# Kernel tuning notes

Hardware: AMD Instinct MI355X
Metric: run time of the kernel (lower is better)

## Reference

```python
import jax, jax.numpy as jnp
import numpy as np

N_NODES = 50000
N_EDGES = 800000
D_IN = 128
D_OUT = 128


def setup_inputs() -> dict:
    key = jax.random.key(0)
    k1, k2, k3, k4, k5 = jax.random.split(key, 5)
    x = jax.random.normal(k1, (N_NODES, D_IN), dtype=jnp.float32)
    src = jax.random.randint(k2, (N_EDGES,), 0, N_NODES, dtype=jnp.int32)
    dst = jax.random.randint(k3, (N_EDGES,), 0, N_NODES, dtype=jnp.int32)
    # nn.Linear(in_feats, out_feats): weight [out, in], bias [out]
    W = jax.random.normal(k4, (D_OUT, D_IN), dtype=jnp.float32) / np.sqrt(D_IN)
    b = jax.random.normal(k5, (D_OUT,), dtype=jnp.float32) * 0.01
    return {"x": x, "src": src, "dst": dst, "W": W, "b": b}


def reference(x, src, dst, W, b):
    # copy_u('h','m') + sum reduce: h_dst = sum_{e:(u->v)} x[u]
    msgs = x[src]  # [E, D_IN] gather of source features
    h = jax.ops.segment_sum(msgs, dst, num_segments=N_NODES)  # [N, D_IN]
    # linear: h @ W.T + b ; dropout_rate=0.0 -> identity
    out = jnp.einsum('nd,od->no', h, W) + b
    return out
```

## Files before the change

kernel.cpp:

```cpp
#include <hip/hip_runtime.h>

#define N_NODES 50000
#define N_EDGES 800000
#define D 128
#define NB 782
#define SORT_CAP 2048

typedef __attribute__((ext_vector_type(8))) short bf16x8;
typedef __attribute__((ext_vector_type(4))) float floatx4;

__device__ __forceinline__ unsigned short f2bf(float f) {
  unsigned u = __builtin_bit_cast(unsigned, f);
  unsigned r = u + 0x7FFFu + ((u >> 16) & 1u);
  return (unsigned short)(r >> 16);
}
__device__ __forceinline__ float bf2f_lo(unsigned u) {
  return __builtin_bit_cast(float, u << 16);
}
__device__ __forceinline__ float bf2f_hi(unsigned u) {
  return __builtin_bit_cast(float, u & 0xFFFF0000u);
}

#define BIN_T 512
#define BIN_CHUNK 3200
#define BIN_BLOCKS 250

__global__ __launch_bounds__(BIN_T) void bin_agg(
    const int* __restrict__ src, const int* __restrict__ dst,
    int* __restrict__ bcursor, unsigned* __restrict__ ebuf, int cap) {
  __shared__ unsigned stage[BIN_CHUNK];
  __shared__ unsigned short stageb[BIN_CHUNK];
  __shared__ int hcnt[NB];
  __shared__ int hstart[NB];
  __shared__ int hcur[NB];
  __shared__ int hgbase[NB];
  __shared__ int wsums[8];

  int t = threadIdx.x;
  int e0 = blockIdx.x * BIN_CHUNK;
  for (int i = t; i < NB; i += BIN_T) hcnt[i] = 0;
  __syncthreads();

  unsigned pk[7];
  short bk[7];
#pragma unroll
  for (int j = 0; j < 7; ++j) {
    int idx = j * BIN_T + t;
    bk[j] = -1;
    if (idx < BIN_CHUNK) {
      int e = e0 + idx;
      int d = dst[e];
      int s = src[e];
      pk[j] = ((unsigned)s << 6) | (unsigned)(d & 63);
      bk[j] = (short)(d >> 6);
      atomicAdd(&hcnt[d >> 6], 1);
    }
  }
  __syncthreads();

  int i0 = 2 * t, i1 = 2 * t + 1;
  int c0 = (i0 < NB) ? hcnt[i0] : 0;
  int c1 = (i1 < NB) ? hcnt[i1] : 0;
  int s2 = c0 + c1;
  int incl = s2;
  int lane = t & 63, wid = t >> 6;
#pragma unroll
  for (int off = 1; off < 64; off <<= 1) {
    int n = __shfl_up(incl, off);
    if (lane >= off) incl += n;
  }
  if (lane == 63) wsums[wid] = incl;
  __syncthreads();
  int wbase = 0;
  for (int w2 = 0; w2 < wid; ++w2) wbase += wsums[w2];
  int base = wbase + incl - s2;
  if (i0 < NB) { hstart[i0] = base;      hcur[i0] = base; }
  if (i1 < NB) { hstart[i1] = base + c0; hcur[i1] = base + c0; }
  __syncthreads();

  for (int i = t; i < NB; i += BIN_T) {
    int c = hcnt[i];
    hgbase[i] = c ? atomicAdd(&bcursor[i * 16], c) : 0;
  }
#pragma unroll
  for (int j = 0; j < 7; ++j) {
    if (bk[j] >= 0) {
      int p = atomicAdd(&hcur[bk[j]], 1);
      stage[p] = pk[j];
      stageb[p] = (unsigned short)bk[j];
    }
  }
  __syncthreads();

  for (int i = t; i < BIN_CHUNK; i += BIN_T) {
    int b = stageb[i];
    int g = hgbase[b] + (i - hstart[b]);
    if (g < cap) ebuf[(size_t)b * cap + g] = stage[i];
  }
}

#define LDA 136
__global__ __launch_bounds__(256) void gemm_xw(
    const float* __restrict__ x, const float* __restrict__ W,
    unsigned short* __restrict__ y) {
  __shared__ unsigned short As[64 * LDA];
  __shared__ unsigned short Ws[128 * LDA];

  int t = threadIdx.x;
  int row0 = blockIdx.x * 64;

  for (int i = t; i < 2048; i += 256) {
    int r = i >> 5;
    int c4 = (i & 31) * 4;
    int gr = row0 + r;
    float4 v = (gr < N_NODES) ? *(const float4*)(x + (size_t)gr * D + c4)
                              : float4{0.f, 0.f, 0.f, 0.f};
    unsigned short* p = &As[r * LDA + c4];
    p[0] = f2bf(v.x); p[1] = f2bf(v.y); p[2] = f2bf(v.z); p[3] = f2bf(v.w);
  }
  for (int i = t; i < 4096; i += 256) {
    int r = i >> 5;
    int c4 = (i & 31) * 4;
    float4 wv = *(const float4*)(W + (size_t)r * D + c4);
    unsigned short* q = &Ws[r * LDA + c4];
    q[0] = f2bf(wv.x); q[1] = f2bf(wv.y); q[2] = f2bf(wv.z); q[3] = f2bf(wv.w);
  }
  __syncthreads();

  int w = t >> 6;
  int lane = t & 63;
  int ln = lane & 15;
  int quad = lane >> 4;

  floatx4 acc[8];
#pragma unroll
  for (int n = 0; n < 8; ++n) acc[n] = floatx4{0.f, 0.f, 0.f, 0.f};

#pragma unroll
  for (int ks = 0; ks < 4; ++ks) {
    int kc = ks * 32 + quad * 8;
    bf16x8 a = *(const bf16x8*)&As[(w * 16 + ln) * LDA + kc];
#pragma unroll
    for (int n = 0; n < 8; ++n) {
      bf16x8 bf = *(const bf16x8*)&Ws[(n * 16 + ln) * LDA + kc];
      acc[n] = __builtin_amdgcn_mfma_f32_16x16x32_bf16(a, bf, acc[n], 0, 0, 0);
    }
  }

  int gr0 = row0 + w * 16 + quad * 4;
#pragma unroll
  for (int n = 0; n < 8; ++n) {
    int gc = n * 16 + ln;
#pragma unroll
    for (int r = 0; r < 4; ++r) {
      int gr = gr0 + r;
      if (gr < N_NODES) y[(size_t)gr * D + gc] = f2bf(acc[n][r]);
    }
  }
}

__global__ __launch_bounds__(256) void gather_sorted(
    const unsigned short* __restrict__ y, const unsigned* __restrict__ ebuf,
    const int* __restrict__ bcursor, const float* __restrict__ bias,
    float* __restrict__ out, int cap) {
  __shared__ int cnts[64];
  __shared__ int curs[64];
  __shared__ int starts[65];
  __shared__ int sorted[SORT_CAP];

  int b = blockIdx.x;
  int t = threadIdx.x;
  if (t < 64) cnts[t] = 0;
  __syncthreads();

  int cnt = bcursor[b * 16];
  if (cnt > cap) cnt = cap;
  if (cnt > SORT_CAP) cnt = SORT_CAP;
  const unsigned* eb = ebuf + (size_t)b * cap;

  for (int i = t; i < cnt; i += 256) atomicAdd(&cnts[eb[i] & 63u], 1);
  __syncthreads();

  if (t < 64) {
    int c = cnts[t];
    int v = c;
#pragma unroll
    for (int off = 1; off < 64; off <<= 1) {
      int n = __shfl_up(v, off);
      if (t >= off) v += n;
    }
    starts[t] = v - c;
    curs[t] = v - c;
    if (t == 63) starts[64] = v;
  }
  __syncthreads();

  for (int i = t; i < cnt; i += 256) {
    unsigned u = eb[i];
    int p = atomicAdd(&curs[u & 63u], 1);
    sorted[p] = (int)(u >> 6);
  }
  __syncthreads();

  int wv = t >> 6;
  int lane = t & 63;
  int g = lane >> 4;
  int l = lane & 15;
  for (int n = wv; n < 64; n += 4) {
    int node = b * 64 + n;
    int beg = starts[n];
    int end = starts[n + 1];
    float acc[8] = {0.f, 0.f, 0.f, 0.f, 0.f, 0.f, 0.f, 0.f};
    int i = beg + g;
    for (; i + 12 < end; i += 16) {
      int s0 = sorted[i];
      int s1 = sorted[i + 4];
      int s2 = sorted[i + 8];
      int s3 = sorted[i + 12];
      uint4 u0 = *(const uint4*)(y + (size_t)s0 * D + l * 8);
      uint4 u1 = *(const uint4*)(y + (size_t)s1 * D + l * 8);
      uint4 u2 = *(const uint4*)(y + (size_t)s2 * D + l * 8);
      uint4 u3 = *(const uint4*)(y + (size_t)s3 * D + l * 8);
      acc[0] += (bf2f_lo(u0.x) + bf2f_lo(u1.x)) + (bf2f_lo(u2.x) + bf2f_lo(u3.x));
      acc[1] += (bf2f_hi(u0.x) + bf2f_hi(u1.x)) + (bf2f_hi(u2.x) + bf2f_hi(u3.x));
      acc[2] += (bf2f_lo(u0.y) + bf2f_lo(u1.y)) + (bf2f_lo(u2.y) + bf2f_lo(u3.y));
      acc[3] += (bf2f_hi(u0.y) + bf2f_hi(u1.y)) + (bf2f_hi(u2.y) + bf2f_hi(u3.y));
      acc[4] += (bf2f_lo(u0.z) + bf2f_lo(u1.z)) + (bf2f_lo(u2.z) + bf2f_lo(u3.z));
      acc[5] += (bf2f_hi(u0.z) + bf2f_hi(u1.z)) + (bf2f_hi(u2.z) + bf2f_hi(u3.z));
      acc[6] += (bf2f_lo(u0.w) + bf2f_lo(u1.w)) + (bf2f_lo(u2.w) + bf2f_lo(u3.w));
      acc[7] += (bf2f_hi(u0.w) + bf2f_hi(u1.w)) + (bf2f_hi(u2.w) + bf2f_hi(u3.w));
    }
    for (; i < end; i += 4) {
      int s = sorted[i];
      uint4 u = *(const uint4*)(y + (size_t)s * D + l * 8);
      acc[0] += bf2f_lo(u.x); acc[1] += bf2f_hi(u.x);
      acc[2] += bf2f_lo(u.y); acc[3] += bf2f_hi(u.y);
      acc[4] += bf2f_lo(u.z); acc[5] += bf2f_hi(u.z);
      acc[6] += bf2f_lo(u.w); acc[7] += bf2f_hi(u.w);
    }
#pragma unroll
    for (int j = 0; j < 8; ++j) {
      acc[j] += __shfl_xor(acc[j], 16);
      acc[j] += __shfl_xor(acc[j], 32);
    }
    if (g == 0 && node < N_NODES) {
      const float* bp = bias + l * 8;
      float4 r0 = {acc[0] + bp[0], acc[1] + bp[1], acc[2] + bp[2], acc[3] + bp[3]};
      float4 r1 = {acc[4] + bp[4], acc[5] + bp[5], acc[6] + bp[6], acc[7] + bp[7]};
      float* op = out + (size_t)node * D + l * 8;
      *(float4*)op = r0;
      *(float4*)(op + 4) = r1;
    }
  }
}

__global__ __launch_bounds__(256) void hist_kernel(
    const int* __restrict__ dst, int* __restrict__ counts) {
  int e = blockIdx.x * 256 + threadIdx.x;
  if (e < N_EDGES) atomicAdd(&counts[dst[e]], 1);
}

#define SBLK 196
__global__ __launch_bounds__(256) void reduce_kernel(
    const int* __restrict__ counts, int* __restrict__ blockSums) {
  int i = blockIdx.x * 256 + threadIdx.x;
  int v = (i < N_NODES) ? counts[i] : 0;
#pragma unroll
  for (int off = 32; off; off >>= 1) v += __shfl_down(v, off);
  __shared__ int ws[4];
  int lane = threadIdx.x & 63, wid = threadIdx.x >> 6;
  if (lane == 0) ws[wid] = v;
  __syncthreads();
  if (threadIdx.x == 0) blockSums[blockIdx.x] = ws[0] + ws[1] + ws[2] + ws[3];
}

__global__ __launch_bounds__(256) void scan_kernel2(
    const int* __restrict__ counts, const int* __restrict__ blockSums,
    int* __restrict__ offsets, int* __restrict__ cursor) {
  int b = blockIdx.x;
  int t = threadIdx.x;
  int lane = t & 63, wid = t >> 6;
  int pv = (t < b) ? blockSums[t] : 0;
#pragma unroll
  for (int off = 32; off; off >>= 1) pv += __shfl_down(pv, off);
  __shared__ int ws[4];
  __shared__ int wsum[4];
  __shared__ int base_s;
  if (lane == 0) ws[wid] = pv;
  __syncthreads();
  if (t == 0) base_s = ws[0] + ws[1] + ws[2] + ws[3];
  int i = b * 256 + t;
  int c = (i < N_NODES) ? counts[i] : 0;
  int v = c;
#pragma unroll
  for (int off = 1; off < 64; off <<= 1) {
    int n = __shfl_up(v, off);
    if (lane >= off) v += n;
  }
  if (lane == 63) wsum[wid] = v;
  __syncthreads();
  int wbase = 0;
  for (int w2 = 0; w2 < wid; ++w2) wbase += wsum[w2];
  int excl = base_s + wbase + v - c;
  if (i < N_NODES) {
    offsets[i] = excl;
    cursor[i] = excl;
    if (i == N_NODES - 1) offsets[N_NODES] = excl + c;
  }
}

__global__ __launch_bounds__(256) void fill_kernel(
    const int* __restrict__ src, const int* __restrict__ dst,
    int* __restrict__ cursor, int* __restrict__ esrc) {
  int e = blockIdx.x * 256 + threadIdx.x;
  if (e >= N_EDGES) return;
  int pos = atomicAdd(&cursor[dst[e]], 1);
  esrc[pos] = src[e];
}

__global__ __launch_bounds__(256) void gather_ybf_kernel(
    const unsigned short* __restrict__ y, const int* __restrict__ esrc,
    const int* __restrict__ offsets, const float* __restrict__ bias,
    float* __restrict__ out) {
  int node = blockIdx.x * 4 + (threadIdx.x >> 6);
  if (node >= N_NODES) return;
  int lane = threadIdx.x & 63;
  int g = lane >> 4;
  int l = lane & 15;
  int beg = offsets[node];
  int end = offsets[node + 1];
  float acc[8] = {0.f, 0.f, 0.f, 0.f, 0.f, 0.f, 0.f, 0.f};
  int i = beg + g;
  for (; i + 4 < end; i += 8) {
    int s0 = esrc[i];
    int s1 = esrc[i + 4];
    uint4 u0 = *(const uint4*)(y + (size_t)s0 * D + l * 8);
    uint4 u1 = *(const uint4*)(y + (size_t)s1 * D + l * 8);
    acc[0] += bf2f_lo(u0.x) + bf2f_lo(u1.x);
    acc[1] += bf2f_hi(u0.x) + bf2f_hi(u1.x);
    acc[2] += bf2f_lo(u0.y) + bf2f_lo(u1.y);
    acc[3] += bf2f_hi(u0.y) + bf2f_hi(u1.y);
    acc[4] += bf2f_lo(u0.z) + bf2f_lo(u1.z);
    acc[5] += bf2f_hi(u0.z) + bf2f_hi(u1.z);
    acc[6] += bf2f_lo(u0.w) + bf2f_lo(u1.w);
    acc[7] += bf2f_hi(u0.w) + bf2f_hi(u1.w);
  }
  if (i < end) {
    int s = esrc[i];
    uint4 u = *(const uint4*)(y + (size_t)s * D + l * 8);
    acc[0] += bf2f_lo(u.x); acc[1] += bf2f_hi(u.x);
    acc[2] += bf2f_lo(u.y); acc[3] += bf2f_hi(u.y);
    acc[4] += bf2f_lo(u.z); acc[5] += bf2f_hi(u.z);
    acc[6] += bf2f_lo(u.w); acc[7] += bf2f_hi(u.w);
  }
#pragma unroll
  for (int j = 0; j < 8; ++j) {
    acc[j] += __shfl_xor(acc[j], 16);
    acc[j] += __shfl_xor(acc[j], 32);
  }
  if (g == 0) {
    const float* bp = bias + l * 8;
    float4 r0 = {acc[0] + bp[0], acc[1] + bp[1], acc[2] + bp[2], acc[3] + bp[3]};
    float4 r1 = {acc[4] + bp[4], acc[5] + bp[5], acc[6] + bp[6], acc[7] + bp[7]};
    float* op = out + (size_t)node * D + l * 8;
    *(float4*)op = r0;
    *(float4*)(op + 4) = r1;
  }
}

__global__ __launch_bounds__(256) void scatter_kernel(
    const float* __restrict__ x, const int* __restrict__ src,
    const int* __restrict__ dst, float* __restrict__ out) {
  int gtid = blockIdx.x * 256 + threadIdx.x;
  int e = gtid >> 6;
  int lane = threadIdx.x & 63;
  if (e >= N_EDGES) return;
  float2 v = ((const float2*)(x + (size_t)src[e] * D))[lane];
  float* orow = out + (size_t)dst[e] * D + lane * 2;
  atomicAdd(orow + 0, v.x);
  atomicAdd(orow + 1, v.y);
}

__global__ __launch_bounds__(256) void transform_kernel(
    float* __restrict__ out, const float* __restrict__ W,
    const float* __restrict__ bias) {
  constexpr int RPB = 64;
  constexpr int HP = 132;
  __shared__ float Hs[RPB][HP];
  int t = threadIdx.x;
  int row0 = blockIdx.x * RPB;
  int nr = min(RPB, N_NODES - row0);
  {
    const float4* g = (const float4*)(out + (size_t)row0 * D);
    for (int i = t; i < nr * (D / 4); i += 256) {
      int r = i >> 5;
      int c = (i & 31) * 4;
      *(float4*)&Hs[r][c] = g[i];
    }
  }
  __syncthreads();
  int tx = t & 15;
  int ty = t >> 4;
  int r0 = ty * 4;
  for (int half = 0; half < 2; ++half) {
    int oc0 = half * 64 + tx * 4;
    const float* Wb = W + (size_t)oc0 * D;
    float4 a0 = {0.f, 0.f, 0.f, 0.f}, a1 = {0.f, 0.f, 0.f, 0.f};
    float4 a2 = {0.f, 0.f, 0.f, 0.f}, a3 = {0.f, 0.f, 0.f, 0.f};
#pragma unroll 8
    for (int k = 0; k < D; k += 4) {
      float4 w0 = *(const float4*)(Wb + 0 * D + k);
      float4 w1 = *(const float4*)(Wb + 1 * D + k);
      float4 w2 = *(const float4*)(Wb + 2 * D + k);
      float4 w3 = *(const float4*)(Wb + 3 * D + k);
      float4 h0 = *(const float4*)&Hs[r0 + 0][k];
      float4 h1 = *(const float4*)&Hs[r0 + 1][k];
      float4 h2 = *(const float4*)&Hs[r0 + 2][k];
      float4 h3 = *(const float4*)&Hs[r0 + 3][k];
#define DOT(hv, wv) fmaf((hv).w, (wv).w, fmaf((hv).z, (wv).z, fmaf((hv).y, (wv).y, (hv).x * (wv).x)))
      a0.x += DOT(h0, w0); a0.y += DOT(h0, w1); a0.z += DOT(h0, w2); a0.w += DOT(h0, w3);
      a1.x += DOT(h1, w0); a1.y += DOT(h1, w1); a1.z += DOT(h1, w2); a1.w += DOT(h1, w3);
      a2.x += DOT(h2, w0); a2.y += DOT(h2, w1); a2.z += DOT(h2, w2); a2.w += DOT(h2, w3);
      a3.x += DOT(h3, w0); a3.y += DOT(h3, w1); a3.z += DOT(h3, w2); a3.w += DOT(h3, w3);
#undef DOT
    }
    float4 bv = *(const float4*)(bias + oc0);
    a0.x += bv.x; a0.y += bv.y; a0.z += bv.z; a0.w += bv.w;
    a1.x += bv.x; a1.y += bv.y; a1.z += bv.z; a1.w += bv.w;
    a2.x += bv.x; a2.y += bv.y; a2.z += bv.z; a2.w += bv.w;
    a3.x += bv.x; a3.y += bv.y; a3.z += bv.z; a3.w += bv.w;
    if (r0 + 0 < nr) *(float4*)(out + (size_t)(row0 + r0 + 0) * D + oc0) = a0;
    if (r0 + 1 < nr) *(float4*)(out + (size_t)(row0 + r0 + 1) * D + oc0) = a1;
    if (r0 + 2 < nr) *(float4*)(out + (size_t)(row0 + r0 + 2) * D + oc0) = a2;
    if (r0 + 3 < nr) *(float4*)(out + (size_t)(row0 + r0 + 3) * D + oc0) = a3;
  }
}

extern "C" void kernel_launch(void* const* d_in, const int* in_sizes, int n_in,
                              void* d_out, int out_size, void* d_ws, size_t ws_size,
                              hipStream_t stream) {
  const float* x = (const float*)d_in[0];
  const int* src = (const int*)d_in[1];
  const int* dst = (const int*)d_in[2];
  const float* W = (const float*)d_in[3];
  const float* b = (const float*)d_in[4];
  float* out = (float*)d_out;

  const size_t ybytes = (size_t)N_NODES * D * sizeof(unsigned short);
  const size_t bcbytes = (size_t)NB * 16 * sizeof(int);

  long long avail = (long long)ws_size - (long long)ybytes - (long long)bcbytes;
  int cap = 0;
  if (avail > 0) {
    long long c = avail / (4LL * NB);
    cap = (c > SORT_CAP) ? SORT_CAP : (int)c;
  }

  if (cap >= 1344) {
    unsigned short* y = (unsigned short*)d_ws;
    int* bcursor = (int*)((char*)d_ws + ybytes);
    unsigned* ebuf = (unsigned*)((char*)bcursor + bcbytes);

    hipMemsetAsync(bcursor, 0, bcbytes, stream);
    bin_agg<<<BIN_BLOCKS, BIN_T, 0, stream>>>(src, dst, bcursor, ebuf, cap);
    gemm_xw<<<NB, 256, 0, stream>>>(x, W, y);
    gather_sorted<<<NB, 256, 0, stream>>>(y, ebuf, bcursor, b, out, cap);
    return;
  }

  const size_t A = 50048;
  const size_t head_ints = 3 * A + 256 + (size_t)N_EDGES;
  const size_t need_csr = head_ints * sizeof(int) + ybytes;

  if (ws_size >= need_csr) {
    int* counts     = (int*)d_ws;
    int* offsets    = counts + A;
    int* cursor     = offsets + A;
    int* blockSums  = cursor + A;
    int* esrc       = blockSums + 256;
    unsigned short* y = (unsigned short*)(esrc + N_EDGES);

    hipMemsetAsync(counts, 0, N_NODES * sizeof(int), stream);
    hist_kernel<<<(N_EDGES + 255) / 256, 256, 0, stream>>>(dst, counts);
    reduce_kernel<<<SBLK, 256, 0, stream>>>(counts, blockSums);
    scan_kernel2<<<SBLK, 256, 0, stream>>>(counts, blockSums, offsets, cursor);
    fill_kernel<<<(N_EDGES + 255) / 256, 256, 0, stream>>>(src, dst, cursor, esrc);
    gemm_xw<<<NB, 256, 0, stream>>>(x, W, y);
    gather_ybf_kernel<<<(N_NODES + 3) / 4, 256, 0, stream>>>(y, esrc, offsets, b, out);
  } else {
    hipMemsetAsync(out, 0, (size_t)N_NODES * D * sizeof(float), stream);
    scatter_kernel<<<N_EDGES / 4, 256, 0, stream>>>(x, src, dst, out);
    transform_kernel<<<(N_NODES + 63) / 64, 256, 0, stream>>>(out, W, b);
  }
}
```

Measured before the change: 152.8 us.

## Fuse edge binning and bf16 GEMM into one heterogeneous prep kernel

Merges the bin_agg and gemm_xw launches into a single prep_kernel whose first NB blocks do the x·W^T MFMA GEMM and whose remaining blocks bin edges by destination block, sharing LDS through a union. The binning blocks are resized to 256 threads and 2048 edges each. The aim is to remove one kernel launch and its serialization and let the independent GEMM and binning work overlap across CUs. The standalone gemm_xw is kept for the fallback path. The union sizes LDS for the larger GEMM layout, which may lower occupancy of the binning blocks.

Result: no change. 150.4 us (-1.6%).

```diff
diff --git a/kernel.cpp b/kernel.cpp
--- a/kernel.cpp
+++ b/kernel.cpp
@@ -21,140 +21,163 @@
   return __builtin_bit_cast(float, u & 0xFFFF0000u);
 }
 
-#define BIN_T 512
-#define BIN_CHUNK 3200
-#define BIN_BLOCKS 250
-
-__global__ __launch_bounds__(BIN_T) void bin_agg(
+#define LDA 136
+#define BIN_T 256
+#define BIN_CHUNK 2048
+#define BIN_BLOCKS 391
+
+struct BinShm {
+  unsigned stage[BIN_CHUNK];
+  unsigned short stageb[BIN_CHUNK];
+  int hcnt[NB];
+  int hstart[NB];
+  int hcur[NB];
+  int hgbase[NB];
+  int wsums[4];
+  int tot;
+};
+struct GemmShm {
+  unsigned short As[64 * LDA];
+  unsigned short Ws[128 * LDA];
+};
+union PrepShm {
+  BinShm bin;
+  GemmShm gemm;
+};
+
+__global__ __launch_bounds__(256) void prep_kernel(
+    const float* __restrict__ x, const float* __restrict__ W,
+    unsigned short* __restrict__ y,
     const int* __restrict__ src, const int* __restrict__ dst,
     int* __restrict__ bcursor, unsigned* __restrict__ ebuf, int cap) {
-  __shared__ unsigned stage[BIN_CHUNK];
-  __shared__ unsigned short stageb[BIN_CHUNK];
-  __shared__ int hcnt[NB];
-  __shared__ int hstart[NB];
-  __shared__ int hcur[NB];
-  __shared__ int hgbase[NB];
-  __shared__ int wsums[8];
-
+  __shared__ PrepShm shm;
   int t = threadIdx.x;
-  int e0 = blockIdx.x * BIN_CHUNK;
-  for (int i = t; i < NB; i += BIN_T) hcnt[i] = 0;
-  __syncthreads();
-
-  unsigned pk[7];
-  short bk[7];
-#pragma unroll
-  for (int j = 0; j < 7; ++j) {
-    int idx = j * BIN_T + t;
-    bk[j] = -1;
-    if (idx < BIN_CHUNK) {
-      int e = e0 + idx;
-      int d = dst[e];
-      int s = src[e];
-      pk[j] = ((unsigned)s << 6) | (unsigned)(d & 63);
-      bk[j] = (short)(d >> 6);
-      atomicAdd(&hcnt[d >> 6], 1);
-    }
-  }
-  __syncthreads();
-
-  int i0 = 2 * t, i1 = 2 * t + 1;
-  int c0 = (i0 < NB) ? hcnt[i0] : 0;
-  int c1 = (i1 < NB) ? hcnt[i1] : 0;
-  int s2 = c0 + c1;
-  int incl = s2;
-  int lane = t & 63, wid = t >> 6;
-#pragma unroll
-  for (int off = 1; off < 64; off <<= 1) {
-    int n = __shfl_up(incl, off);
-    if (lane >= off) incl += n;
-  }
-  if (lane == 63) wsums[wid] = incl;
-  __syncthreads();
-  int wbase = 0;
-  for (int w2 = 0; w2 < wid; ++w2) wbase += wsums[w2];
-  int base = wbase + incl - s2;
-  if (i0 < NB) { hstart[i0] = base;      hcur[i0] = base; }
-  if (i1 < NB) { hstart[i1] = base + c0; hcur[i1] = base + c0; }
-  __syncthreads();
-
-  for (int i = t; i < NB; i += BIN_T) {
-    int c = hcnt[i];
-    hgbase[i] = c ? atomicAdd(&bcursor[i * 16], c) : 0;
-  }
-#pragma unroll
-  for (int j = 0; j < 7; ++j) {
-    if (bk[j] >= 0) {
-      int p = atomicAdd(&hcur[bk[j]], 1);
-      stage[p] = pk[j];
-      stageb[p] = (unsigned short)bk[j];
-    }
-  }
-  __syncthreads();
-
-  for (int i = t; i < BIN_CHUNK; i += BIN_T) {
-    int b = stageb[i];
-    int g = hgbase[b] + (i - hstart[b]);
-    if (g < cap) ebuf[(size_t)b * cap + g] = stage[i];
-  }
-}
-
-#define LDA 136
-__global__ __launch_bounds__(256) void gemm_xw(
-    const float* __restrict__ x, const float* __restrict__ W,
-    unsigned short* __restrict__ y) {
-  __shared__ unsigned short As[64 * LDA];
-  __shared__ unsigned short Ws[128 * LDA];
-
-  int t = threadIdx.x;
-  int row0 = blockIdx.x * 64;
-
-  for (int i = t; i < 2048; i += 256) {
-    int r = i >> 5;
-    int c4 = (i & 31) * 4;
-    int gr = row0 + r;
-    float4 v = (gr < N_NODES) ? *(const float4*)(x + (size_t)gr * D + c4)
-                              : float4{0.f, 0.f, 0.f, 0.f};
-    unsigned short* p = &As[r * LDA + c4];
-    p[0] = f2bf(v.x); p[1] = f2bf(v.y); p[2] = f2bf(v.z); p[3] = f2bf(v.w);
-  }
-  for (int i = t; i < 4096; i += 256) {
-    int r = i >> 5;
-    int c4 = (i & 31) * 4;
-    float4 wv = *(const float4*)(W + (size_t)r * D + c4);
-    unsigned short* q = &Ws[r * LDA + c4];
-    q[0] = f2bf(wv.x); q[1] = f2bf(wv.y); q[2] = f2bf(wv.z); q[3] = f2bf(wv.w);
-  }
-  __syncthreads();
-
-  int w = t >> 6;
-  int lane = t & 63;
-  int ln = lane & 15;
-  int quad = lane >> 4;
-
-  floatx4 acc[8];
-#pragma unroll
-  for (int n = 0; n < 8; ++n) acc[n] = floatx4{0.f, 0.f, 0.f, 0.f};
-
-#pragma unroll
-  for (int ks = 0; ks < 4; ++ks) {
-    int kc = ks * 32 + quad * 8;
-    bf16x8 a = *(const bf16x8*)&As[(w * 16 + ln) * LDA + kc];
+
+  if (blockIdx.x < NB) {
+    unsigned short* As = shm.gemm.As;
+    unsigned short* Ws = shm.gemm.Ws;
+    int row0 = blockIdx.x * 64;
+
+    for (int i = t; i < 2048; i += 256) {
+      int r = i >> 5;
+      int c4 = (i & 31) * 4;
+      int gr = row0 + r;
+      float4 v = (gr < N_NODES) ? *(const float4*)(x + (size_t)gr * D + c4)
+                                : float4{0.f, 0.f, 0.f, 0.f};
+      unsigned short* p = &As[r * LDA + c4];
+      p[0] = f2bf(v.x); p[1] = f2bf(v.y); p[2] = f2bf(v.z); p[3] = f2bf(v.w);
+    }
+    for (int i = t; i < 4096; i += 256) {
+      int r = i >> 5;
+      int c4 = (i & 31) * 4;
+      float4 wv = *(const float4*)(W + (size_t)r * D + c4);
+      unsigned short* q = &Ws[r * LDA + c4];
+      q[0] = f2bf(wv.x); q[1] = f2bf(wv.y); q[2] = f2bf(wv.z); q[3] = f2bf(wv.w);
+    }
+    __syncthreads();
+
+    int w = t >> 6;
+    int lane = t & 63;
+    int ln = lane & 15;
+    int quad = lane >> 4;
+
+    floatx4 acc[8];
+#pragma unroll
+    for (int n = 0; n < 8; ++n) acc[n] = floatx4{0.f, 0.f, 0.f, 0.f};
+
+#pragma unroll
+    for (int ks = 0; ks < 4; ++ks) {
+      int kc = ks * 32 + quad * 8;
+      bf16x8 a = *(const bf16x8*)&As[(w * 16 + ln) * LDA + kc];
+#pragma unroll
+      for (int n = 0; n < 8; ++n) {
+        bf16x8 bf = *(const bf16x8*)&Ws[(n * 16 + ln) * LDA + kc];
+        acc[n] = __builtin_amdgcn_mfma_f32_16x16x32_bf16(a, bf, acc[n], 0, 0, 0);
+      }
+    }
+
+    int gr0 = row0 + w * 16 + quad * 4;
 #pragma unroll
     for (int n = 0; n < 8; ++n) {
-      bf16x8 bf = *(const bf16x8*)&Ws[(n * 16 + ln) * LDA + kc];
-      acc[n] = __builtin_amdgcn_mfma_f32_16x16x32_bf16(a, bf, acc[n], 0, 0, 0);
-    }
-  }
-
-  int gr0 = row0 + w * 16 + quad * 4;
-#pragma unroll
-  for (int n = 0; n < 8; ++n) {
-    int gc = n * 16 + ln;
-#pragma unroll
-    for (int r = 0; r < 4; ++r) {
-      int gr = gr0 + r;
-      if (gr < N_NODES) y[(size_t)gr * D + gc] = f2bf(acc[n][r]);
+      int gc = n * 16 + ln;
+#pragma unroll
+      for (int r = 0; r < 4; ++r) {
+        int gr = gr0 + r;
+        if (gr < N_NODES) y[(size_t)gr * D + gc] = f2bf(acc[n][r]);
+      }
+    }
+  } else {
+    BinShm& B = shm.bin;
+    int blk = blockIdx.x - NB;
+    int e0 = blk * BIN_CHUNK;
+    for (int i = t; i < NB; i += BIN_T) B.hcnt[i] = 0;
+    __syncthreads();
+
+    unsigned pk[8];
+    short bk[8];
+#pragma unroll
+    for (int j = 0; j < 8; ++j) {
+      int e = e0 + j * BIN_T + t;
+      bk[j] = -1;
+      if (e < N_EDGES) {
+        int d = dst[e];
+        int s = src[e];
+        pk[j] = ((unsigned)s << 6) | (unsigned)(d & 63);
+        bk[j] = (short)(d >> 6);
+        atomicAdd(&B.hcnt[d >> 6], 1);
+      }
+    }
+    __syncthreads();
+
+    int c4[4];
+    int s4 = 0;
+    int base4 = t * 4;
+#pragma unroll
+    for (int j = 0; j < 4; ++j) {
+      int idx = base4 + j;
+      c4[j] = (idx < NB) ? B.hcnt[idx] : 0;
+      s4 += c4[j];
+    }
+    int incl = s4;
+    int lane = t & 63, wid = t >> 6;
+#pragma unroll
+    for (int off = 1; off < 64; off <<= 1) {
+      int n = __shfl_up(incl, off);
+      if (lane >= off) incl += n;
+    }
+    if (lane == 63) B.wsums[wid] = incl;
+    __syncthreads();
+    int wbase = 0;
+    for (int w2 = 0; w2 < wid; ++w2) wbase += B.wsums[w2];
+    int run = wbase + incl - s4;
+#pragma unroll
+    for (int j = 0; j < 4; ++j) {
+      int idx = base4 + j;
+      if (idx < NB) { B.hstart[idx] = run; B.hcur[idx] = run; }
+      run += c4[j];
+    }
+    if (t == BIN_T - 1) B.tot = run;
+    __syncthreads();
+
+    for (int i = t; i < NB; i += BIN_T) {
+      int c = B.hcnt[i];
+      B.hgbase[i] = c ? atomicAdd(&bcursor[i * 16], c) : 0;
+    }
+#pragma unroll
+    for (int j = 0; j < 8; ++j) {
+      if (bk[j] >= 0) {
+        int p = atomicAdd(&B.hcur[bk[j]], 1);
+        B.stage[p] = pk[j];
+        B.stageb[p] = (unsigned short)bk[j];
+      }
+    }
+    __syncthreads();
+
+    int tot = B.tot;
+    for (int i = t; i < tot; i += BIN_T) {
+      int b = B.stageb[i];
+      int g = B.hgbase[b] + (i - B.hstart[b]);
+      if (g < cap) ebuf[(size_t)b * cap + g] = B.stage[i];
     }
   }
 }
@@ -318,6 +341,59 @@
   esrc[pos] = src[e];
 }
 
+__global__ __launch_bounds__(256) void gemm_xw(
+    const float* __restrict__ x, const float* __restrict__ W,
+    unsigned short* __restrict__ y) {
+  __shared__ unsigned short As[64 * LDA];
+  __shared__ unsigned short Ws[128 * LDA];
+  int t = threadIdx.x;
+  int row0 = blockIdx.x * 64;
+  for (int i = t; i < 2048; i += 256) {
+    int r = i >> 5;
+    int c4 = (i & 31) * 4;
+    int gr = row0 + r;
+    float4 v = (gr < N_NODES) ? *(const float4*)(x + (size_t)gr * D + c4)
+                              : float4{0.f, 0.f, 0.f, 0.f};
+    unsigned short* p = &As[r * LDA + c4];
+    p[0] = f2bf(v.x); p[1] = f2bf(v.y); p[2] = f2bf(v.z); p[3] = f2bf(v.w);
+  }
+  for (int i = t; i < 4096; i += 256) {
+    int r = i >> 5;
+    int c4 = (i & 31) * 4;
+    float4 wv = *(const float4*)(W + (size_t)r * D + c4);
+    unsigned short* q = &Ws[r * LDA + c4];
+    q[0] = f2bf(wv.x); q[1] = f2bf(wv.y); q[2] = f2bf(wv.z); q[3] = f2bf(wv.w);
+  }
+  __syncthreads();
+  int w = t >> 6;
+  int lane = t & 63;
+  int ln = lane & 15;
+  int quad = lane >> 4;
+  floatx4 acc[8];
+#pragma unroll
+  for (int n = 0; n < 8; ++n) acc[n] = floatx4{0.f, 0.f, 0.f, 0.f};
+#pragma unroll
+  for (int ks = 0; ks < 4; ++ks) {
+    int kc = ks * 32 + quad * 8;
+    bf16x8 a = *(const bf16x8*)&As[(w * 16 + ln) * LDA + kc];
+#pragma unroll
+    for (int n = 0; n < 8; ++n) {
+      bf16x8 bf = *(const bf16x8*)&Ws[(n * 16 + ln) * LDA + kc];
+      acc[n] = __builtin_amdgcn_mfma_f32_16x16x32_bf16(a, bf, acc[n], 0, 0, 0);
+    }
+  }
+  int gr0 = row0 + w * 16 + quad * 4;
+#pragma unroll
+  for (int n = 0; n < 8; ++n) {
+    int gc = n * 16 + ln;
+#pragma unroll
+    for (int r = 0; r < 4; ++r) {
+      int gr = gr0 + r;
+      if (gr < N_NODES) y[(size_t)gr * D + gc] = f2bf(acc[n][r]);
+    }
+  }
+}
+
 __global__ __launch_bounds__(256) void gather_ybf_kernel(
     const unsigned short* __restrict__ y, const int* __restrict__ esrc,
     const int* __restrict__ offsets, const float* __restrict__ bias,
@@ -462,8 +538,8 @@
     unsigned* ebuf = (unsigned*)((char*)bcursor + bcbytes);
 
     hipMemsetAsync(bcursor, 0, bcbytes, stream);
-    bin_agg<<<BIN_BLOCKS, BIN_T, 0, stream>>>(src, dst, bcursor, ebuf, cap);
-    gemm_xw<<<NB, 256, 0, stream>>>(x, W, y);
+    prep_kernel<<<NB + BIN_BLOCKS, 256, 0, stream>>>(x, W, y, src, dst,
+                                                     bcursor, ebuf, cap);
     gather_sorted<<<NB, 256, 0, stream>>>(y, ebuf, bcursor, b, out, cap);
     return;
   }
```
